# Performance work log

Hardware: AMD Instinct MI355X
Metric: run time of the kernel (lower is better)

Reference implementation:

```python
import jax, jax.numpy as jnp
import numpy as np

B, T, D, H = 4, 2048, 1024, 16
HD = D // H  # head_dim = 64

def setup_inputs() -> dict:
    key = jax.random.key(0)
    k1, k2, k3 = jax.random.split(key, 3)
    s = 1.0 / np.sqrt(D)
    x = jax.random.normal(k1, (B, T, D), dtype=jnp.float32)
    W_qkv = jax.random.normal(k2, (D, 3 * D), dtype=jnp.float32) * s
    W_proj = jax.random.normal(k3, (D, D), dtype=jnp.float32) * s
    return {"x": x, "W_qkv": W_qkv, "W_proj": W_proj}

def reference(x, W_qkv, W_proj):
    Bq, Tq, C = x.shape
    qkv = x @ W_qkv                                   # [B,T,3C]
    q, k, v = jnp.split(qkv, 3, axis=-1)
    def heads(t):  # [B,T,C] -> [B,H,T,HD]
        return t.reshape(Bq, Tq, H, HD).transpose(0, 2, 1, 3)
    q, k, v = heads(q), heads(k), heads(v)
    scale = 1.0 / np.sqrt(HD)
    att = jnp.einsum('bhqd,bhkd->bhqk', q, k) * scale  # [B,H,T,T]
    causal = jnp.tril(jnp.ones((Tq, Tq), dtype=bool))
    att = jnp.where(causal[None, None], att, -jnp.inf)
    att = jax.nn.softmax(att, axis=-1)
    y = jnp.einsum('bhqk,bhkd->bhqd', att, v)          # [B,H,T,HD]
    y = y.transpose(0, 2, 1, 3).reshape(Bq, Tq, C)
    return y @ W_proj
```

## Files before the change

### kernel.cpp

```cpp
#include <hip/hip_runtime.h>

typedef unsigned short ushort_t;
typedef __attribute__((ext_vector_type(8))) __bf16 bf16x8;
typedef __attribute__((ext_vector_type(4))) float f32x4;
typedef __attribute__((ext_vector_type(16))) float f32x16;
typedef __attribute__((ext_vector_type(4))) float float4v;
typedef __attribute__((ext_vector_type(8))) unsigned short ushort8v;
typedef __attribute__((ext_vector_type(4))) unsigned short ushort4v;
typedef __attribute__((ext_vector_type(4))) unsigned uint4v;

#define T_LEN 2048
#define D_DIM 1024
#define NHEAD 16
#define HDIM 64
#define BH 64
#define MROWS 8192
#define PERQKV ((size_t)BH * T_LEN * HDIM)

__device__ __forceinline__ ushort_t f2bf(float f) {
  unsigned u = __builtin_bit_cast(unsigned, f);
  u = (u + 0x7FFFu + ((u >> 16) & 1u)) >> 16;
  return (ushort_t)u;
}

__device__ __forceinline__ float fast_exp2(float x) {
  float r; asm("v_exp_f32 %0, %1" : "=v"(r) : "v"(x)); return r;
}

__device__ __forceinline__ void load_lds16(const ushort_t* g, ushort_t* l) {
  __builtin_amdgcn_global_load_lds((const __attribute__((address_space(1))) void*)g,
                                   (__attribute__((address_space(3))) void*)l, 16, 0, 0);
}

__global__ __launch_bounds__(256) void k_cvt_x(const float* __restrict__ x,
                                               ushort_t* __restrict__ xb) {
  int i = blockIdx.x * 256 + threadIdx.x;
  float4v v = ((const float4v*)x)[i];
  ushort4v o;
  o[0] = f2bf(v[0]); o[1] = f2bf(v[1]); o[2] = f2bf(v[2]); o[3] = f2bf(v[3]);
  ((ushort4v*)xb)[i] = o;
}

__global__ __launch_bounds__(256) void k_transpose(const float* __restrict__ W,
                                                   ushort_t* __restrict__ Wt,
                                                   int R, int C) {
  __shared__ ushort_t tile[32][33];
  int tx = threadIdx.x & 31, ty = threadIdx.x >> 5;
  int r0 = blockIdx.y << 5, c0 = blockIdx.x << 5;
#pragma unroll
  for (int i = 0; i < 4; ++i) {
    int r = ty + i * 8;
    tile[r][tx] = f2bf(W[(size_t)(r0 + r) * C + c0 + tx]);
  }
  __syncthreads();
#pragma unroll
  for (int i = 0; i < 4; ++i) {
    int r = ty + i * 8;
    Wt[(size_t)(c0 + r) * R + r0 + tx] = tile[tx][r];
  }
}

template <int N, int K, int EPI>
__global__ __launch_bounds__(256) void k_gemm(const ushort_t* __restrict__ A,
                                              const ushort_t* __restrict__ Bt,
                                              ushort_t* __restrict__ O16,
                                              float* __restrict__ O32) {
  __shared__ __align__(16) ushort_t Atile[128 * 32];
  __shared__ __align__(16) ushort_t Btile[128 * 32];
  const int tid = threadIdx.x;
  const int lane = tid & 63, w = tid >> 6;
  const int g = lane >> 4, c = lane & 15;
  const int wm = w >> 1, wn = w & 1;
  const int m0 = blockIdx.y * 128, n0 = blockIdx.x * 128;

  f32x4 acc[4][4];
#pragma unroll
  for (int i = 0; i < 4; ++i)
#pragma unroll
    for (int j = 0; j < 4; ++j) acc[i][j] = (f32x4){0.f, 0.f, 0.f, 0.f};

  for (int k0 = 0; k0 < K; k0 += 32) {
    __syncthreads();
#pragma unroll
    for (int r = 0; r < 2; ++r) {
      int flat = r * 256 + tid;
      int row = flat >> 2, slot = flat & 3;
      int gsl = slot ^ (row & 3);
      load_lds16(A + (size_t)(m0 + row) * K + k0 + gsl * 8,
                 &Atile[(r * 256 + w * 64) * 8]);
      load_lds16(Bt + (size_t)(n0 + row) * K + k0 + gsl * 8,
                 &Btile[(r * 256 + w * 64) * 8]);
    }
    __syncthreads();

    bf16x8 af[4], bfr[4];
#pragma unroll
    for (int mi = 0; mi < 4; ++mi) {
      int row = wm * 64 + mi * 16 + c;
      int sl = g ^ (row & 3);
      af[mi] = *(const bf16x8*)&Atile[row * 32 + sl * 8];
    }
#pragma unroll
    for (int ni = 0; ni < 4; ++ni) {
      int row = wn * 64 + ni * 16 + c;
      int sl = g ^ (row & 3);
      bfr[ni] = *(const bf16x8*)&Btile[row * 32 + sl * 8];
    }
#pragma unroll
    for (int mi = 0; mi < 4; ++mi)
#pragma unroll
      for (int ni = 0; ni < 4; ++ni)
        acc[mi][ni] = __builtin_amdgcn_mfma_f32_16x16x32_bf16(af[mi], bfr[ni],
                                                              acc[mi][ni], 0, 0, 0);
  }

#pragma unroll
  for (int mi = 0; mi < 4; ++mi)
#pragma unroll
    for (int ni = 0; ni < 4; ++ni) {
      int n = n0 + wn * 64 + ni * 16 + c;
#pragma unroll
      for (int j = 0; j < 4; ++j) {
        int m = m0 + wm * 64 + mi * 16 + g * 4 + j;
        float v = acc[mi][ni][j];
        if constexpr (EPI == 0) {
          int which = n >> 10, hn = n & 1023;
          int h = hn >> 6, d = hn & 63;
          int b = m >> 11, t = m & 2047;
          if (which == 0) v *= 0.18033688f;
          O16[(size_t)which * PERQKV +
              (((size_t)(b * NHEAD + h) * T_LEN + t) * HDIM + d)] = f2bf(v);
        } else {
          O32[(size_t)m * N + n] = v;
        }
      }
    }
}

__global__ __launch_bounds__(128) void k_attn(const ushort_t* __restrict__ Q,
                                              const ushort_t* __restrict__ Kv,
                                              const ushort_t* __restrict__ Vv,
                                              ushort_t* __restrict__ Y) {
  __shared__ __align__(16) ushort_t Kt[2][64 * 64];
  __shared__ __align__(16) ushort_t Vt[2][64 * 64];

  const int bid = blockIdx.x;
  const int bh = (bid & 7) * 8 + ((bid >> 3) & 7);
  const int p = 31 - (bid >> 6);
  const int nkt = p + 1;

  const int tid = threadIdx.x, lane = tid & 63, w = tid >> 6;
  const int hi = lane >> 5, lc = lane & 31;
  const int q32 = p * 64 + w * 32;
  const size_t base = (size_t)bh * (T_LEN * HDIM);

  bf16x8 qf[4];
#pragma unroll
  for (int st = 0; st < 4; ++st)
    qf[st] = *(const bf16x8*)(Q + base + (size_t)(q32 + lc) * HDIM + st * 16 + hi * 8);

  f32x16 o0, o1;
#pragma unroll
  for (int i = 0; i < 16; ++i) { o0[i] = 0.f; o1[i] = 0.f; }
  float mrun = 0.f, lrun = 0.f;

  const int ksl = tid & 7, krow0 = tid >> 3;
  const int kpair = tid & 31, vk0 = 2 * kpair, vd0 = (tid >> 5) * 8;

  bf16x8 kreg[4];
  ushort8v vreg[4];
  auto stage_issue = [&](int kt) {
    const ushort_t* kb = Kv + base + (size_t)kt * 64 * HDIM;
    const ushort_t* vb = Vv + base + (size_t)kt * 64 * HDIM;
    vreg[0] = *(const ushort8v*)(vb + (size_t)vk0 * HDIM + vd0);
    vreg[1] = *(const ushort8v*)(vb + (size_t)(vk0 + 1) * HDIM + vd0);
    vreg[2] = *(const ushort8v*)(vb + (size_t)vk0 * HDIM + vd0 + 32);
    vreg[3] = *(const ushort8v*)(vb + (size_t)(vk0 + 1) * HDIM + vd0 + 32);
#pragma unroll
    for (int m = 0; m < 4; ++m)
      kreg[m] = *(const bf16x8*)(kb + (size_t)(krow0 + 16 * m) * HDIM + ksl * 8);
  };
  auto stage_write = [&](int buf) {
#pragma unroll
    for (int m = 0; m < 4; ++m) {
      int r = krow0 + 16 * m;
      *(bf16x8*)&Kt[buf][r * 64 + ((ksl ^ (r & 7)) << 3)] = kreg[m];
    }
#pragma unroll
    for (int e = 0; e < 8; ++e) {
      int rd = vd0 + e;
      unsigned pv = (unsigned)vreg[0][e] | ((unsigned)vreg[1][e] << 16);
      *(unsigned*)&Vt[buf][rd * 64 + (((kpair >> 2) ^ (rd & 7)) << 3) + 2 * (kpair & 3)] = pv;
      int rd2 = rd + 32;
      unsigned pv2 = (unsigned)vreg[2][e] | ((unsigned)vreg[3][e] << 16);
      *(unsigned*)&Vt[buf][rd2 * 64 + (((kpair >> 2) ^ (rd2 & 7)) << 3) + 2 * (kpair & 3)] = pv2;
    }
  };

  stage_issue(0); stage_write(0);
  if (nkt > 1) stage_issue(1);
  __syncthreads();

  for (int kt = 0; kt < nkt; ++kt) {
    const int cur = kt & 1;
    const ushort_t* kbuf = &Kt[cur][0];
    const ushort_t* vbuf = &Vt[cur][0];

    f32x16 s0, s1;
#pragma unroll
    for (int i = 0; i < 16; ++i) { s0[i] = 0.f; s1[i] = 0.f; }
#pragma unroll
    for (int st = 0; st < 4; ++st) {
      bf16x8 kf0 = *(const bf16x8*)&kbuf[lc * 64 + (((2 * st + hi) ^ (lc & 7)) << 3)];
      s0 = __builtin_amdgcn_mfma_f32_32x32x16_bf16(kf0, qf[st], s0, 0, 0, 0);
    }
#pragma unroll
    for (int st = 0; st < 4; ++st) {
      bf16x8 kf1 = *(const bf16x8*)&kbuf[(32 + lc) * 64 + (((2 * st + hi) ^ (lc & 7)) << 3)];
      s1 = __builtin_amdgcn_mfma_f32_32x32x16_bf16(kf1, qf[st], s1, 0, 0, 0);
    }

    if (kt * 64 + 63 > q32) {
      const int q = q32 + lc;
#pragma unroll
      for (int r = 0; r < 16; ++r) {
        int cr = (r & 3) + 8 * (r >> 2) + 4 * hi;
        if (kt * 64 + cr > q)      s0[r] = -3.0e38f;
        if (kt * 64 + 32 + cr > q) s1[r] = -3.0e38f;
      }
    }

    float tm[8];
#pragma unroll
    for (int i = 0; i < 8; ++i) tm[i] = fmaxf(fmaxf(s0[i], s0[i + 8]), fmaxf(s1[i], s1[i + 8]));
#pragma unroll
    for (int i = 0; i < 4; ++i) tm[i] = fmaxf(tm[i], tm[i + 4]);
    float tmax = fmaxf(fmaxf(tm[0], tm[1]), fmaxf(tm[2], tm[3]));
    tmax = fmaxf(tmax, __shfl_xor(tmax, 32));

    if (!__all(tmax <= mrun + 11.0f)) {
      float mnew = fmaxf(mrun, tmax);
      float sc = fast_exp2(mrun - mnew);
      lrun *= sc; mrun = mnew;
#pragma unroll
      for (int r = 0; r < 16; ++r) {
        int cr = (r & 3) + 8 * (r >> 2) + 4 * hi;
        float scr = __shfl(sc, cr);
        o0[r] *= scr; o1[r] *= scr;
      }
    }

#pragma unroll
    for (int r = 0; r < 16; ++r) s0[r] = fast_exp2(s0[r] - mrun);
#pragma unroll
    for (int r = 0; r < 16; ++r) s1[r] = fast_exp2(s1[r] - mrun);
    {
      float u0 = 0.f, u1 = 0.f, u2 = 0.f, u3 = 0.f;
#pragma unroll
      for (int i = 0; i < 4; ++i) {
        u0 += s0[i];     u1 += s0[i + 4];  u2 += s0[i + 8];  u3 += s0[i + 12];
        u0 += s1[i];     u1 += s1[i + 4];  u2 += s1[i + 8];  u3 += s1[i + 12];
      }
      lrun += (u0 + u1) + (u2 + u3);
    }

    unsigned wv[16];
#pragma unroll
    for (int i = 0; i < 8; ++i) {
      asm("v_cvt_pk_bf16_f32 %0, %1, %2" : "=v"(wv[i])     : "v"(s0[2 * i]), "v"(s0[2 * i + 1]));
      asm("v_cvt_pk_bf16_f32 %0, %1, %2" : "=v"(wv[8 + i]) : "v"(s1[2 * i]), "v"(s1[2 * i + 1]));
    }
    bf16x8 pf[4];
#pragma unroll
    for (int g4 = 0; g4 < 4; ++g4) {
      unsigned a0 = wv[4 * g4], a1 = wv[4 * g4 + 1];
      unsigned a2 = wv[4 * g4 + 2], a3 = wv[4 * g4 + 3];
      asm("v_permlane32_swap_b32 %0, %1" : "+v"(a0), "+v"(a2));
      asm("v_permlane32_swap_b32 %0, %1" : "+v"(a1), "+v"(a3));
      uint4v fw; fw[0] = a0; fw[1] = a1; fw[2] = a2; fw[3] = a3;
      pf[g4] = __builtin_bit_cast(bf16x8, fw);
    }

#pragma unroll
    for (int km = 0; km < 4; ++km) {
      int gsl = ((2 * km + hi) ^ (lc & 7)) << 3;
      bf16x8 vb0 = *(const bf16x8*)&vbuf[lc * 64 + gsl];
      bf16x8 vb1 = *(const bf16x8*)&vbuf[(32 + lc) * 64 + gsl];
      o0 = __builtin_amdgcn_mfma_f32_32x32x16_bf16(pf[km], vb0, o0, 0, 0, 0);
      o1 = __builtin_amdgcn_mfma_f32_32x32x16_bf16(pf[km], vb1, o1, 0, 0, 0);
    }

    if (kt + 1 < nkt) stage_write((kt + 1) & 1);
    if (kt + 2 < nkt) stage_issue(kt + 2);
    __syncthreads();
  }

  float lt = lrun + __shfl_xor(lrun, 32);
  float invl = 1.f / lt;
  const int b_ = bh >> 4, h_ = bh & 15;
#pragma unroll
  for (int r = 0; r < 16; ++r) {
    int cr = (r & 3) + 8 * (r >> 2) + 4 * hi;
    float iv = __shfl(invl, cr);
    size_t m = (size_t)b_ * T_LEN + q32 + cr;
    Y[m * D_DIM + h_ * HDIM + lc]      = f2bf(o0[r] * iv);
    Y[m * D_DIM + h_ * HDIM + 32 + lc] = f2bf(o1[r] * iv);
  }
}

extern "C" void kernel_launch(void* const* d_in, const int* in_sizes, int n_in,
                              void* d_out, int out_size, void* d_ws, size_t ws_size,
                              hipStream_t stream) {
  const float* x     = (const float*)d_in[0];
  const float* Wqkv  = (const float*)d_in[1];
  const float* Wproj = (const float*)d_in[2];
  float* out = (float*)d_out;
  ushort_t* ws = (ushort_t*)d_ws;

  ushort_t* Xb  = ws;
  ushort_t* WqT = Xb  + (size_t)MROWS * D_DIM;
  ushort_t* WpT = WqT + (size_t)3 * D_DIM * D_DIM;
  ushort_t* Qb  = WpT + (size_t)D_DIM * D_DIM;
  ushort_t* Kb  = Qb + PERQKV;
  ushort_t* Vb  = Kb + PERQKV;
  ushort_t* Yb  = Vb + PERQKV;

  k_cvt_x<<<(MROWS * D_DIM / 4) / 256, 256, 0, stream>>>(x, Xb);
  k_transpose<<<dim3(3 * D_DIM / 32, D_DIM / 32), 256, 0, stream>>>(Wqkv, WqT, D_DIM, 3 * D_DIM);
  k_transpose<<<dim3(D_DIM / 32, D_DIM / 32), 256, 0, stream>>>(Wproj, WpT, D_DIM, D_DIM);
  k_gemm<3 * D_DIM, D_DIM, 0><<<dim3(3 * D_DIM / 128, MROWS / 128), 256, 0, stream>>>(Xb, WqT, Qb, nullptr);
  k_attn<<<2048, 128, 0, stream>>>(Qb, Kb, Vb, Yb);
  k_gemm<D_DIM, D_DIM, 1><<<dim3(D_DIM / 128, MROWS / 128), 256, 0, stream>>>(Yb, WpT, nullptr, out);
}
```

Measured before the change: 189.6 us.

## Single-buffer attention K/V tiles, load K via direct-to-LDS, add MFMA priority

Removes the K/V double buffers in LDS and loads K straight into shared memory with a global-to-LDS load helper, skipping the register round trip. V is still staged through registers, but its load is issued at the top of the iteration, one tile ahead. s_setprio is raised around the MFMA blocks. The aim is to cut LDS footprint and VGPR use so more blocks fit per CU, and to favour matrix issue. The cost is an extra barrier per iteration and less overlap, since the K load and V write now sit between two syncs.

```diff
diff --git a/kernel.cpp b/kernel.cpp
--- a/kernel.cpp
+++ b/kernel.cpp
@@ -141,8 +141,8 @@
                                               const ushort_t* __restrict__ Kv,
                                               const ushort_t* __restrict__ Vv,
                                               ushort_t* __restrict__ Y) {
-  __shared__ __align__(16) ushort_t Kt[2][64 * 64];
-  __shared__ __align__(16) ushort_t Vt[2][64 * 64];
+  __shared__ __align__(16) ushort_t Kt[64 * 64];
+  __shared__ __align__(16) ushort_t Vt[64 * 64];
 
   const int bid = blockIdx.x;
   const int bh = (bid & 7) * 8 + ((bid >> 3) & 7);
@@ -164,61 +164,60 @@
   for (int i = 0; i < 16; ++i) { o0[i] = 0.f; o1[i] = 0.f; }
   float mrun = 0.f, lrun = 0.f;
 
-  const int ksl = tid & 7, krow0 = tid >> 3;
+  const int krow_g = w * 8 + (lane >> 3);
+  const int ksrc_off = (((lane & 7) ^ (krow_g & 7)) << 3);
+  auto stage_K = [&](int kt) {
+    const ushort_t* kb = Kv + base + (size_t)kt * 64 * HDIM;
+#pragma unroll
+    for (int m = 0; m < 4; ++m)
+      load_lds16(kb + (size_t)(m * 16 + krow_g) * HDIM + ksrc_off,
+                 &Kt[(m * 128 + w * 64) * 8]);
+  };
+
   const int kpair = tid & 31, vk0 = 2 * kpair, vd0 = (tid >> 5) * 8;
-
-  bf16x8 kreg[4];
   ushort8v vreg[4];
-  auto stage_issue = [&](int kt) {
-    const ushort_t* kb = Kv + base + (size_t)kt * 64 * HDIM;
+  auto issue_V = [&](int kt) {
     const ushort_t* vb = Vv + base + (size_t)kt * 64 * HDIM;
     vreg[0] = *(const ushort8v*)(vb + (size_t)vk0 * HDIM + vd0);
     vreg[1] = *(const ushort8v*)(vb + (size_t)(vk0 + 1) * HDIM + vd0);
     vreg[2] = *(const ushort8v*)(vb + (size_t)vk0 * HDIM + vd0 + 32);
     vreg[3] = *(const ushort8v*)(vb + (size_t)(vk0 + 1) * HDIM + vd0 + 32);
-#pragma unroll
-    for (int m = 0; m < 4; ++m)
-      kreg[m] = *(const bf16x8*)(kb + (size_t)(krow0 + 16 * m) * HDIM + ksl * 8);
   };
-  auto stage_write = [&](int buf) {
-#pragma unroll
-    for (int m = 0; m < 4; ++m) {
-      int r = krow0 + 16 * m;
-      *(bf16x8*)&Kt[buf][r * 64 + ((ksl ^ (r & 7)) << 3)] = kreg[m];
-    }
+  auto write_V = [&]() {
 #pragma unroll
     for (int e = 0; e < 8; ++e) {
       int rd = vd0 + e;
       unsigned pv = (unsigned)vreg[0][e] | ((unsigned)vreg[1][e] << 16);
-      *(unsigned*)&Vt[buf][rd * 64 + (((kpair >> 2) ^ (rd & 7)) << 3) + 2 * (kpair & 3)] = pv;
+      *(unsigned*)&Vt[rd * 64 + (((kpair >> 2) ^ (rd & 7)) << 3) + 2 * (kpair & 3)] = pv;
       int rd2 = rd + 32;
       unsigned pv2 = (unsigned)vreg[2][e] | ((unsigned)vreg[3][e] << 16);
-      *(unsigned*)&Vt[buf][rd2 * 64 + (((kpair >> 2) ^ (rd2 & 7)) << 3) + 2 * (kpair & 3)] = pv2;
+      *(unsigned*)&Vt[rd2 * 64 + (((kpair >> 2) ^ (rd2 & 7)) << 3) + 2 * (kpair & 3)] = pv2;
     }
   };
 
-  stage_issue(0); stage_write(0);
-  if (nkt > 1) stage_issue(1);
+  stage_K(0);
+  issue_V(0);
+  write_V();
   __syncthreads();
 
   for (int kt = 0; kt < nkt; ++kt) {
-    const int cur = kt & 1;
-    const ushort_t* kbuf = &Kt[cur][0];
-    const ushort_t* vbuf = &Vt[cur][0];
+    if (kt + 1 < nkt) issue_V(kt + 1);
 
     f32x16 s0, s1;
 #pragma unroll
     for (int i = 0; i < 16; ++i) { s0[i] = 0.f; s1[i] = 0.f; }
+    __builtin_amdgcn_s_setprio(1);
 #pragma unroll
     for (int st = 0; st < 4; ++st) {
-      bf16x8 kf0 = *(const bf16x8*)&kbuf[lc * 64 + (((2 * st + hi) ^ (lc & 7)) << 3)];
+      bf16x8 kf0 = *(const bf16x8*)&Kt[lc * 64 + (((2 * st + hi) ^ (lc & 7)) << 3)];
       s0 = __builtin_amdgcn_mfma_f32_32x32x16_bf16(kf0, qf[st], s0, 0, 0, 0);
     }
 #pragma unroll
     for (int st = 0; st < 4; ++st) {
-      bf16x8 kf1 = *(const bf16x8*)&kbuf[(32 + lc) * 64 + (((2 * st + hi) ^ (lc & 7)) << 3)];
+      bf16x8 kf1 = *(const bf16x8*)&Kt[(32 + lc) * 64 + (((2 * st + hi) ^ (lc & 7)) << 3)];
       s1 = __builtin_amdgcn_mfma_f32_32x32x16_bf16(kf1, qf[st], s1, 0, 0, 0);
     }
+    __builtin_amdgcn_s_setprio(0);
 
     if (kt * 64 + 63 > q32) {
       const int q = q32 + lc;
@@ -281,17 +280,19 @@
       pf[g4] = __builtin_bit_cast(bf16x8, fw);
     }
 
+    __builtin_amdgcn_s_setprio(1);
 #pragma unroll
     for (int km = 0; km < 4; ++km) {
       int gsl = ((2 * km + hi) ^ (lc & 7)) << 3;
-      bf16x8 vb0 = *(const bf16x8*)&vbuf[lc * 64 + gsl];
-      bf16x8 vb1 = *(const bf16x8*)&vbuf[(32 + lc) * 64 + gsl];
+      bf16x8 vb0 = *(const bf16x8*)&Vt[lc * 64 + gsl];
+      bf16x8 vb1 = *(const bf16x8*)&Vt[(32 + lc) * 64 + gsl];
       o0 = __builtin_amdgcn_mfma_f32_32x32x16_bf16(pf[km], vb0, o0, 0, 0, 0);
       o1 = __builtin_amdgcn_mfma_f32_32x32x16_bf16(pf[km], vb1, o1, 0, 0, 0);
     }
-
-    if (kt + 1 < nkt) stage_write((kt + 1) & 1);
-    if (kt + 2 < nkt) stage_issue(kt + 2);
+    __builtin_amdgcn_s_setprio(0);
+
+    __syncthreads();
+    if (kt + 1 < nkt) { stage_K(kt + 1); write_V(); }
     __syncthreads();
   }
 
```

Result: no change. 190.0 us (+0.2%).

## Pair heavy and light causal query tiles per attention block, add MFMA priority

Applied to the files above, without the earlier changes.

Each attention block now handles two query tiles, the long tile pA=31-i followed by the short tile pB=i, so every block does the same 33 KV iterations. The grid is halved to 1024 blocks and the K/V double-buffer pipeline runs straight across the tile switch. It also raises wave priority around the MFMA sections with s_setprio and adds a launch-bounds occupancy hint. This aims to remove tail imbalance from causal masking, at the cost of fewer blocks and a mid-loop epilogue plus Q reload.

```diff
diff --git a/kernel.cpp b/kernel.cpp
--- a/kernel.cpp
+++ b/kernel.cpp
@@ -137,23 +137,25 @@
     }
 }
 
-__global__ __launch_bounds__(128) void k_attn(const ushort_t* __restrict__ Q,
-                                              const ushort_t* __restrict__ Kv,
-                                              const ushort_t* __restrict__ Vv,
-                                              ushort_t* __restrict__ Y) {
+__global__ __launch_bounds__(128, 4) void k_attn(const ushort_t* __restrict__ Q,
+                                                 const ushort_t* __restrict__ Kv,
+                                                 const ushort_t* __restrict__ Vv,
+                                                 ushort_t* __restrict__ Y) {
   __shared__ __align__(16) ushort_t Kt[2][64 * 64];
   __shared__ __align__(16) ushort_t Vt[2][64 * 64];
 
   const int bid = blockIdx.x;
   const int bh = (bid & 7) * 8 + ((bid >> 3) & 7);
-  const int p = 31 - (bid >> 6);
-  const int nkt = p + 1;
+  const int pairidx = bid >> 6;
+  const int pA = 31 - pairidx, pB = pairidx;
+  const int nktA = pA + 1;
+  const int total = nktA + pB + 1;
 
   const int tid = threadIdx.x, lane = tid & 63, w = tid >> 6;
   const int hi = lane >> 5, lc = lane & 31;
-  const int q32 = p * 64 + w * 32;
   const size_t base = (size_t)bh * (T_LEN * HDIM);
 
+  int q32 = pA * 64 + w * 32;
   bf16x8 qf[4];
 #pragma unroll
   for (int st = 0; st < 4; ++st)
@@ -197,18 +199,44 @@
     }
   };
 
+  const int b_ = bh >> 4, h_ = bh & 15;
+  auto epilogue = [&]() {
+    float lt = lrun + __shfl_xor(lrun, 32);
+    float invl = 1.f / lt;
+#pragma unroll
+    for (int r = 0; r < 16; ++r) {
+      int cr = (r & 3) + 8 * (r >> 2) + 4 * hi;
+      float iv = __shfl(invl, cr);
+      size_t m = (size_t)b_ * T_LEN + q32 + cr;
+      Y[m * D_DIM + h_ * HDIM + lc]      = f2bf(o0[r] * iv);
+      Y[m * D_DIM + h_ * HDIM + 32 + lc] = f2bf(o1[r] * iv);
+    }
+  };
+
   stage_issue(0); stage_write(0);
-  if (nkt > 1) stage_issue(1);
+  stage_issue(1);
   __syncthreads();
 
-  for (int kt = 0; kt < nkt; ++kt) {
-    const int cur = kt & 1;
+  for (int it = 0; it < total; ++it) {
+    if (it == nktA) {
+      epilogue();
+      q32 = pB * 64 + w * 32;
+#pragma unroll
+      for (int st = 0; st < 4; ++st)
+        qf[st] = *(const bf16x8*)(Q + base + (size_t)(q32 + lc) * HDIM + st * 16 + hi * 8);
+#pragma unroll
+      for (int i = 0; i < 16; ++i) { o0[i] = 0.f; o1[i] = 0.f; }
+      mrun = 0.f; lrun = 0.f;
+    }
+    const int kt = (it < nktA) ? it : it - nktA;
+    const int cur = it & 1;
     const ushort_t* kbuf = &Kt[cur][0];
     const ushort_t* vbuf = &Vt[cur][0];
 
     f32x16 s0, s1;
 #pragma unroll
     for (int i = 0; i < 16; ++i) { s0[i] = 0.f; s1[i] = 0.f; }
+    __builtin_amdgcn_s_setprio(1);
 #pragma unroll
     for (int st = 0; st < 4; ++st) {
       bf16x8 kf0 = *(const bf16x8*)&kbuf[lc * 64 + (((2 * st + hi) ^ (lc & 7)) << 3)];
@@ -219,6 +247,7 @@
       bf16x8 kf1 = *(const bf16x8*)&kbuf[(32 + lc) * 64 + (((2 * st + hi) ^ (lc & 7)) << 3)];
       s1 = __builtin_amdgcn_mfma_f32_32x32x16_bf16(kf1, qf[st], s1, 0, 0, 0);
     }
+    __builtin_amdgcn_s_setprio(0);
 
     if (kt * 64 + 63 > q32) {
       const int q = q32 + lc;
@@ -281,6 +310,7 @@
       pf[g4] = __builtin_bit_cast(bf16x8, fw);
     }
 
+    __builtin_amdgcn_s_setprio(1);
 #pragma unroll
     for (int km = 0; km < 4; ++km) {
       int gsl = ((2 * km + hi) ^ (lc & 7)) << 3;
@@ -289,23 +319,17 @@
       o0 = __builtin_amdgcn_mfma_f32_32x32x16_bf16(pf[km], vb0, o0, 0, 0, 0);
       o1 = __builtin_amdgcn_mfma_f32_32x32x16_bf16(pf[km], vb1, o1, 0, 0, 0);
     }
-
-    if (kt + 1 < nkt) stage_write((kt + 1) & 1);
-    if (kt + 2 < nkt) stage_issue(kt + 2);
+    __builtin_amdgcn_s_setprio(0);
+
+    if (it + 1 < total) stage_write((it + 1) & 1);
+    if (it + 2 < total) {
+      int itn = it + 2;
+      stage_issue((itn < nktA) ? itn : itn - nktA);
+    }
     __syncthreads();
   }
 
-  float lt = lrun + __shfl_xor(lrun, 32);
-  float invl = 1.f / lt;
-  const int b_ = bh >> 4, h_ = bh & 15;
-#pragma unroll
-  for (int r = 0; r < 16; ++r) {
-    int cr = (r & 3) + 8 * (r >> 2) + 4 * hi;
-    float iv = __shfl(invl, cr);
-    size_t m = (size_t)b_ * T_LEN + q32 + cr;
-    Y[m * D_DIM + h_ * HDIM + lc]      = f2bf(o0[r] * iv);
-    Y[m * D_DIM + h_ * HDIM + 32 + lc] = f2bf(o1[r] * iv);
-  }
+  epilogue();
 }
 
 extern "C" void kernel_launch(void* const* d_in, const int* in_sizes, int n_in,
@@ -329,6 +353,6 @@
   k_transpose<<<dim3(3 * D_DIM / 32, D_DIM / 32), 256, 0, stream>>>(Wqkv, WqT, D_DIM, 3 * D_DIM);
   k_transpose<<<dim3(D_DIM / 32, D_DIM / 32), 256, 0, stream>>>(Wproj, WpT, D_DIM, D_DIM);
   k_gemm<3 * D_DIM, D_DIM, 0><<<dim3(3 * D_DIM / 128, MROWS / 128), 256, 0, stream>>>(Xb, WqT, Qb, nullptr);
-  k_attn<<<2048, 128, 0, stream>>>(Qb, Kb, Vb, Yb);
+  k_attn<<<1024, 128, 0, stream>>>(Qb, Kb, Vb, Yb);
   k_gemm<D_DIM, D_DIM, 1><<<dim3(D_DIM / 128, MROWS / 128), 256, 0, stream>>>(Yb, WpT, nullptr, out);
 }
```

After: 189.1 us. About the same (-0.3%).
